# Performance work log

Hardware: AMD Instinct MI355X
Metric: run time of the kernel (lower is better)

Reference implementation:

```python
import jax, jax.numpy as jnp
import numpy as np

N_NODES = 100000


def _gcn_norm(edge_index, num_nodes):
    # PyG GCNConv default: add self-loops, symmetric normalization.
    src, dst = edge_index[0], edge_index[1]
    loop = jnp.arange(num_nodes, dtype=src.dtype)
    src = jnp.concatenate([src, loop])
    dst = jnp.concatenate([dst, loop])
    deg = jax.ops.segment_sum(jnp.ones_like(dst, dtype=jnp.float32), dst,
                              num_segments=num_nodes)
    dinv = jnp.where(deg > 0, jax.lax.rsqrt(jnp.maximum(deg, 1.0)), 0.0)
    norm = dinv[src] * dinv[dst]  # [E + N]
    return src, dst, norm


def _gcn_layer(x, src, dst, norm, W, b, num_nodes):
    h = x @ W                              # [N, out]
    msg = h[src] * norm[:, None]           # gather + scale, [E+N, out]
    agg = jax.ops.segment_sum(msg, dst, num_segments=num_nodes)  # scatter-add
    return agg + b


def setup_inputs() -> dict:
    key = jax.random.key(0)
    ks = jax.random.split(key, 12)
    in_c, hid = 64, 128
    dims = [in_c, hid, hid // 2, hid // 4, hid // 8, 1]
    x = jax.random.normal(ks[0], (N_NODES, in_c), dtype=jnp.float32)
    edge_index = jax.random.randint(ks[1], (2, 1600000), 0, N_NODES,
                                    dtype=jnp.int64)
    inp = {"x": x, "edge_index": edge_index}
    for i in range(5):
        fan_in = dims[i]
        s = 1.0 / np.sqrt(fan_in)
        inp[f"W{i+1}"] = jax.random.uniform(ks[2 + 2 * i], (dims[i], dims[i + 1]),
                                            minval=-s, maxval=s,
                                            dtype=jnp.float32)
        inp[f"b{i+1}"] = jnp.zeros((dims[i + 1],), dtype=jnp.float32)
    return inp


def reference(x, edge_index, W1, b1, W2, b2, W3, b3, W4, b4, W5, b5):
    num_nodes = x.shape[0]
    src, dst, norm = _gcn_norm(edge_index, num_nodes)
    h = _gcn_layer(x, src, dst, norm, W1, b1, num_nodes)
    h = jax.nn.relu(h)
    h = _gcn_layer(h, src, dst, norm, W2, b2, num_nodes)
    h = jax.nn.relu(h)
    h = _gcn_layer(h, src, dst, norm, W3, b3, num_nodes)
    h = jax.nn.relu(h)
    h = _gcn_layer(h, src, dst, norm, W4, b4, num_nodes)
    h = jax.nn.relu(h)
    h = _gcn_layer(h, src, dst, norm, W5, b5, num_nodes)
    return h
```

## Files before the change

kernel.cpp:

```cpp
#include <hip/hip_runtime.h>
#include <math.h>


#define NBIN_MAX 256
#define BSHIFT 9
#define BINW 512
#define CHUNK 2048
#define BCAP 12288

__global__ __launch_bounds__(256) void k_init(int* __restrict__ binCur, int nbin) {
    int t = threadIdx.x;
    if (t < nbin) binCur[t] = t * BCAP;
}

__global__ __launch_bounds__(256) void k_binfill(const int* __restrict__ src,
                                                 const int* __restrict__ dst, int E,
                                                 int nbin, int* __restrict__ binCur,
                                                 unsigned* __restrict__ tmp) {
    __shared__ int h[NBIN_MAX];
    __shared__ int res[NBIN_MAX];
    int t = threadIdx.x;
    int e0 = blockIdx.x * CHUNK;
    int e1 = min(e0 + CHUNK, E);
    int vend = e0 + ((e1 - e0) & ~3);
    for (int i = t; i < nbin; i += 256) h[i] = 0;
    __syncthreads();
    for (int e = e0 + t * 4; e < vend; e += 1024) {
        int4 d = *(const int4*)&dst[e];
        atomicAdd(&h[d.x >> BSHIFT], 1);
        atomicAdd(&h[d.y >> BSHIFT], 1);
        atomicAdd(&h[d.z >> BSHIFT], 1);
        atomicAdd(&h[d.w >> BSHIFT], 1);
    }
    for (int e = vend + t; e < e1; e += 256)
        atomicAdd(&h[dst[e] >> BSHIFT], 1);
    __syncthreads();
    for (int i = t; i < nbin; i += 256)
        res[i] = h[i] ? atomicAdd(&binCur[i], h[i]) : 0;
    __syncthreads();
    for (int i = t; i < nbin; i += 256) h[i] = 0;
    __syncthreads();
    for (int e = e0 + t * 4; e < vend; e += 1024) {
        int4 d = *(const int4*)&dst[e];
        int4 s = *(const int4*)&src[e];
        int b0 = d.x >> BSHIFT;
        int p0 = res[b0] + atomicAdd(&h[b0], 1);
        tmp[p0] = ((unsigned)s.x << BSHIFT) | (unsigned)(d.x & (BINW - 1));
        int b1 = d.y >> BSHIFT;
        int p1 = res[b1] + atomicAdd(&h[b1], 1);
        tmp[p1] = ((unsigned)s.y << BSHIFT) | (unsigned)(d.y & (BINW - 1));
        int b2 = d.z >> BSHIFT;
        int p2 = res[b2] + atomicAdd(&h[b2], 1);
        tmp[p2] = ((unsigned)s.z << BSHIFT) | (unsigned)(d.z & (BINW - 1));
        int b3 = d.w >> BSHIFT;
        int p3 = res[b3] + atomicAdd(&h[b3], 1);
        tmp[p3] = ((unsigned)s.w << BSHIFT) | (unsigned)(d.w & (BINW - 1));
    }
    for (int e = vend + t; e < e1; e += 256) {
        int d = dst[e];
        int b = d >> BSHIFT;
        int p = res[b] + atomicAdd(&h[b], 1);
        tmp[p] = ((unsigned)src[e] << BSHIFT) | (unsigned)(d & (BINW - 1));
    }
}

__global__ __launch_bounds__(256) void k_base(const int* __restrict__ binCur,
                                              int nbin, int* __restrict__ binBase) {
    __shared__ int sh[256];
    int t = threadIdx.x;
    int c = (t < nbin) ? (binCur[t] - t * BCAP) : 0;
    sh[t] = c;
    __syncthreads();
    for (int d = 1; d < 256; d <<= 1) {
        int u = (t >= d) ? sh[t - d] : 0;
        __syncthreads();
        sh[t] += u;
        __syncthreads();
    }
    if (t < nbin) binBase[t] = sh[t] - c;
    if (t == nbin - 1) binBase[nbin] = sh[t];
}

__global__ __launch_bounds__(256) void k_csr(const unsigned* __restrict__ tmp,
                                             const int* __restrict__ binBase,
                                             int n, int nbin,
                                             float* __restrict__ dinv,
                                             int* __restrict__ offs,
                                             int* __restrict__ csr) {
    __shared__ int ldeg[BINW];
    __shared__ int loff[BINW];
    __shared__ int pair[256];
    int b = blockIdx.x;
    int t = threadIdx.x;
    ldeg[t] = 0; ldeg[t + 256] = 0;
    __syncthreads();
    int lo = binBase[b];
    int cnt = binBase[b + 1] - lo;
    const unsigned* tb = tmp + (size_t)b * BCAP;
    for (int p = t; p < cnt; p += 256)
        atomicAdd(&ldeg[tb[p] & (BINW - 1u)], 1);
    __syncthreads();
    int a0 = ldeg[2 * t], a1 = ldeg[2 * t + 1];
    pair[t] = a0 + a1;
    __syncthreads();
    int v = pair[t];
    for (int d = 1; d < 256; d <<= 1) {
        int u = (t >= d) ? pair[t - d] : 0;
        __syncthreads();
        pair[t] += u;
        __syncthreads();
    }
    int ex = pair[t] - v;
    loff[2 * t] = ex;
    loff[2 * t + 1] = ex + a0;
    __syncthreads();
    int v0 = b << BSHIFT;
    for (int i = t; i < BINW; i += 256) {
        int vv = v0 + i;
        if (vv < n) {
            offs[vv] = lo + loff[i];
            dinv[vv] = 1.0f / sqrtf((float)(ldeg[i] + 1));
        }
    }
    if (t == 0 && b == nbin - 1) offs[n] = binBase[nbin];
    __syncthreads();
    ldeg[t] = 0; ldeg[t + 256] = 0;
    __syncthreads();
    for (int p = t; p < cnt; p += 256) {
        unsigned u = tb[p];
        int d0 = (int)(u & (BINW - 1u));
        int pos = loff[d0] + atomicAdd(&ldeg[d0], 1);
        csr[lo + pos] = (int)(u >> BSHIFT);
    }
}

template <int W, int DEPTH, bool RELU, bool BIAS, bool L1S>
__global__ __launch_bounds__(256) void k_aggp(const float* __restrict__ S,
                                              const float* __restrict__ dinv,
                                              const int* __restrict__ offs,
                                              const int* __restrict__ csr,
                                              const float* __restrict__ bg,
                                              float* __restrict__ Y, int n) {
    constexpr int LPR = W / 4;
    constexpr int GPW = 64 / LPR;
    int lane = threadIdx.x & 63;
    int wave = threadIdx.x >> 6;
    int grp = lane / LPR;
    int j = lane % LPR;
    int v = blockIdx.x * (4 * GPW) + wave * GPW + grp;
    if (v >= n) return;
    float dv = dinv[v];
    float4 acc0, acc1 = make_float4(0.f, 0.f, 0.f, 0.f);
    {
        float4 sv = *(const float4*)&S[(size_t)v * W + j * 4];
        float sc = L1S ? dv : 1.0f;
        acc0 = make_float4(sv.x * sc, sv.y * sc, sv.z * sc, sv.w * sc);
    }
    int e0 = offs[v], re = offs[v + 1];
    int nb = (re - e0) / DEPTH;
    float4 bA[DEPTH], bB[DEPTH];
    float dA[DEPTH], dB[DEPTH];
    int iA[DEPTH], iB[DEPTH];
    auto loadIdx = [&](int* ix, int base) {
#pragma unroll
        for (int d = 0; d < DEPTH; ++d)
            ix[d] = __builtin_nontemporal_load(&csr[base + d]);
    };
    auto gather = [&](float4* bf, float* ds, const int* ix) {
#pragma unroll
        for (int d = 0; d < DEPTH; ++d) {
            bf[d] = *(const float4*)&S[(size_t)ix[d] * W + j * 4];
            if (L1S) ds[d] = dinv[ix[d]];
        }
    };
    auto consume = [&](const float4* bf, const float* ds) {
#pragma unroll
        for (int d = 0; d < DEPTH; ++d) {
            float sc = L1S ? ds[d] : 1.0f;
            if (d & 1) { acc1.x += bf[d].x * sc; acc1.y += bf[d].y * sc;
                         acc1.z += bf[d].z * sc; acc1.w += bf[d].w * sc; }
            else       { acc0.x += bf[d].x * sc; acc0.y += bf[d].y * sc;
                         acc0.z += bf[d].z * sc; acc0.w += bf[d].w * sc; }
        }
    };
    if (nb >= 1) {
        loadIdx(iA, e0);
        gather(bA, dA, iA);
        if (nb >= 2) loadIdx(iB, e0 + DEPTH);
        int b = 0;
        while (b + 2 <= nb) {
            gather(bB, dB, iB);
            if (b + 2 < nb) loadIdx(iA, e0 + (b + 2) * DEPTH);
            consume(bA, dA);
            if (b + 2 < nb) {
                gather(bA, dA, iA);
                if (b + 3 < nb) loadIdx(iB, e0 + (b + 3) * DEPTH);
            }
            consume(bB, dB);
            b += 2;
        }
        if (b < nb) consume(bA, dA);
    }
    for (int k = e0 + nb * DEPTH; k < re; ++k) {
        int u = __builtin_nontemporal_load(&csr[k]);
        float4 a = *(const float4*)&S[(size_t)u * W + j * 4];
        float sc = L1S ? dinv[u] : 1.0f;
        acc0.x += a.x * sc; acc0.y += a.y * sc; acc0.z += a.z * sc; acc0.w += a.w * sc;
    }
    acc0.x += acc1.x; acc0.y += acc1.y; acc0.z += acc1.z; acc0.w += acc1.w;
    float4 r;
    r.x = dv * acc0.x; r.y = dv * acc0.y; r.z = dv * acc0.z; r.w = dv * acc0.w;
    if (BIAS) {
        float4 bv = *(const float4*)&bg[j * 4];
        r.x += bv.x; r.y += bv.y; r.z += bv.z; r.w += bv.w;
    }
    if (RELU) {
        r.x = fmaxf(r.x, 0.f); r.y = fmaxf(r.y, 0.f);
        r.z = fmaxf(r.z, 0.f); r.w = fmaxf(r.w, 0.f);
    }
    *(float4*)&Y[(size_t)v * W + j * 4] = r;
}

template <int DEPTH>
__global__ __launch_bounds__(256) void k_agg16g5(const float* __restrict__ S,
                                                 const float* __restrict__ dinv,
                                                 const int* __restrict__ offs,
                                                 const int* __restrict__ csr,
                                                 const float* __restrict__ b4,
                                                 const float* __restrict__ W5,
                                                 float* __restrict__ Y, int n) {
    constexpr int W = 16, LPR = 4, GPW = 16;
    int lane = threadIdx.x & 63;
    int wave = threadIdx.x >> 6;
    int grp = lane / LPR;
    int j = lane % LPR;
    int v = blockIdx.x * (4 * GPW) + wave * GPW + grp;
    if (v >= n) return;
    float dv = dinv[v];
    float4 acc0 = *(const float4*)&S[(size_t)v * W + j * 4];
    float4 acc1 = make_float4(0.f, 0.f, 0.f, 0.f);
    int e0 = offs[v], re = offs[v + 1];
    int nb = (re - e0) / DEPTH;
    float4 bA[DEPTH], bB[DEPTH];
    int iA[DEPTH], iB[DEPTH];
    auto loadIdx = [&](int* ix, int base) {
#pragma unroll
        for (int d = 0; d < DEPTH; ++d)
            ix[d] = __builtin_nontemporal_load(&csr[base + d]);
    };
    auto gather = [&](float4* bf, const int* ix) {
#pragma unroll
        for (int d = 0; d < DEPTH; ++d)
            bf[d] = *(const float4*)&S[(size_t)ix[d] * W + j * 4];
    };
    auto consume = [&](const float4* bf) {
#pragma unroll
        for (int d = 0; d < DEPTH; ++d) {
            if (d & 1) { acc1.x += bf[d].x; acc1.y += bf[d].y;
                         acc1.z += bf[d].z; acc1.w += bf[d].w; }
            else       { acc0.x += bf[d].x; acc0.y += bf[d].y;
                         acc0.z += bf[d].z; acc0.w += bf[d].w; }
        }
    };
    if (nb >= 1) {
        loadIdx(iA, e0);
        gather(bA, iA);
        if (nb >= 2) loadIdx(iB, e0 + DEPTH);
        int b = 0;
        while (b + 2 <= nb) {
            gather(bB, iB);
            if (b + 2 < nb) loadIdx(iA, e0 + (b + 2) * DEPTH);
            consume(bA);
            if (b + 2 < nb) {
                gather(bA, iA);
                if (b + 3 < nb) loadIdx(iB, e0 + (b + 3) * DEPTH);
            }
            consume(bB);
            b += 2;
        }
        if (b < nb) consume(bA);
    }
    for (int k = e0 + nb * DEPTH; k < re; ++k) {
        int u = __builtin_nontemporal_load(&csr[k]);
        float4 a = *(const float4*)&S[(size_t)u * W + j * 4];
        acc0.x += a.x; acc0.y += a.y; acc0.z += a.z; acc0.w += a.w;
    }
    acc0.x += acc1.x; acc0.y += acc1.y; acc0.z += acc1.z; acc0.w += acc1.w;
    float4 bv = *(const float4*)&b4[j * 4];
    float4 w5 = *(const float4*)&W5[j * 4];
    float hx = fmaxf(dv * acc0.x + bv.x, 0.f);
    float hy = fmaxf(dv * acc0.y + bv.y, 0.f);
    float hz = fmaxf(dv * acc0.z + bv.z, 0.f);
    float hw = fmaxf(dv * acc0.w + bv.w, 0.f);
    float p = hx * w5.x + hy * w5.y + hz * w5.z + hw * w5.w;
    p += __shfl_xor(p, 1);
    p += __shfl_xor(p, 2);
    if (j == 0) Y[v] = p * dv;
}

__global__ __launch_bounds__(256) void k_agg1(const float* __restrict__ S,
                                              const float* __restrict__ dinv,
                                              const int* __restrict__ offs,
                                              const int* __restrict__ csr,
                                              const float* __restrict__ bg,
                                              float* __restrict__ Y, int n) {
    int v = blockIdx.x * 256 + threadIdx.x;
    if (v >= n) return;
    float s0 = S[v], s1 = 0.f, s2 = 0.f, s3 = 0.f;
    int e = offs[v], re = offs[v + 1];
    for (; e + 4 <= re; e += 4) {
        int i0 = csr[e], i1 = csr[e + 1], i2 = csr[e + 2], i3 = csr[e + 3];
        s0 += S[i0]; s1 += S[i1]; s2 += S[i2]; s3 += S[i3];
    }
    for (; e < re; ++e) s0 += S[csr[e]];
    Y[v] = dinv[v] * ((s0 + s1) + (s2 + s3)) + bg[0];
}

template <int IN, int OUT, int EPI, int NR>
__global__ __launch_bounds__(256) void k_gemm(const float* __restrict__ X,
                                              const float* __restrict__ Wg,
                                              const float* __restrict__ bg,
                                              const float* __restrict__ dinv,
                                              float* __restrict__ Y, int nrows) {
    constexpr int TPR = OUT / 4;
    constexpr int GROUPS = 256 / TPR;
    constexpr int ROWS = GROUPS * NR;
    constexpr int XS = IN + 1;
    __shared__ __align__(16) float Wl[IN * OUT];
    __shared__ float xl[ROWS * XS];
    __shared__ float bl[OUT];
    int tid = threadIdx.x;
    for (int i = tid; i < IN * OUT; i += 256) Wl[i] = Wg[i];
    if (EPI == 0)
        for (int i = tid; i < OUT; i += 256) bl[i] = bg[i];
    int base = blockIdx.x * ROWS;
    for (int i = tid; i < ROWS * IN; i += 256) {
        int r = i / IN, c = i % IN;
        int row = base + r;
        xl[r * XS + c] = (row < nrows) ? X[(size_t)base * IN + i] : 0.0f;
    }
    __syncthreads();
    int g = tid / TPR;
    int c0 = (tid % TPR) * 4;
    float4 acc[NR];
#pragma unroll
    for (int r = 0; r < NR; ++r) acc[r] = make_float4(0.f, 0.f, 0.f, 0.f);
#pragma unroll 8
    for (int k = 0; k < IN; ++k) {
        float4 w = *(const float4*)&Wl[k * OUT + c0];
#pragma unroll
        for (int r = 0; r < NR; ++r) {
            float a = xl[(g * NR + r) * XS + k];
            acc[r].x += a * w.x; acc[r].y += a * w.y;
            acc[r].z += a * w.z; acc[r].w += a * w.w;
        }
    }
#pragma unroll
    for (int r = 0; r < NR; ++r) {
        int row = base + g * NR + r;
        if (row >= nrows) continue;
        float4 o = acc[r];
        if (EPI == 0) {
            o.x = fmaxf(o.x + bl[c0], 0.f);
            o.y = fmaxf(o.y + bl[c0 + 1], 0.f);
            o.z = fmaxf(o.z + bl[c0 + 2], 0.f);
            o.w = fmaxf(o.w + bl[c0 + 3], 0.f);
        } else {
            float d0 = dinv[row];
            o.x *= d0; o.y *= d0; o.z *= d0; o.w *= d0;
        }
        *(float4*)&Y[(size_t)row * OUT + c0] = o;
    }
}

extern "C" void kernel_launch(void* const* d_in, const int* in_sizes, int n_in,
                              void* d_out, int out_size, void* d_ws, size_t ws_size,
                              hipStream_t stream) {
    const float* x  = (const float*)d_in[0];
    const int*   ei = (const int*)d_in[1];
    const float* W1 = (const float*)d_in[2];  const float* b1 = (const float*)d_in[3];
    const float* W2 = (const float*)d_in[4];  const float* b2 = (const float*)d_in[5];
    const float* W3 = (const float*)d_in[6];  const float* b3 = (const float*)d_in[7];
    const float* W4 = (const float*)d_in[8];  const float* b4 = (const float*)d_in[9];
    const float* W5 = (const float*)d_in[10]; const float* b5 = (const float*)d_in[11];

    const int N = in_sizes[0] / 64;
    const int E = in_sizes[1] / 2;
    const int* src = ei;
    const int* dst = ei + E;
    const int nbin = (N + BINW - 1) / BINW;

    char* ws = (char*)d_ws;
    size_t off = 0;
    auto alloc = [&](size_t bytes) -> void* {
        void* p = ws + off;
        off = (off + bytes + 255) & ~(size_t)255;
        return p;
    };
    float* dinv    = (float*)alloc((size_t)N * 4);
    int*   offs    = (int*)alloc((size_t)(N + 1) * 4);
    int*   binBase = (int*)alloc((size_t)(NBIN_MAX + 1) * 4);
    int*   binCur  = (int*)alloc((size_t)NBIN_MAX * 4);
    int*   csr     = (int*)alloc((size_t)E * 4);
    float* s5      = (float*)alloc((size_t)N * 4);
    float* A       = (float*)alloc((size_t)N * 128 * 4);
    float* B       = (float*)alloc((size_t)N * 64 * 4);
    float* C       = (float*)alloc((size_t)N * 64 * 4);
    unsigned* tmp  = (unsigned*)C;

    k_init<<<1, 256, 0, stream>>>(binCur, nbin);
    k_binfill<<<(E + CHUNK - 1) / CHUNK, 256, 0, stream>>>(src, dst, E, nbin, binCur, tmp);
    k_base<<<1, 256, 0, stream>>>(binCur, nbin, binBase);
    k_csr<<<nbin, 256, 0, stream>>>(tmp, binBase, N, nbin, dinv, offs, csr);

    k_aggp<64, 4, false, false, true><<<(N + 15) / 16, 256, 0, stream>>>(x, dinv, offs, csr, nullptr, B, N);
    k_gemm<64, 128, 0, 4><<<(N + 31) / 32, 256, 0, stream>>>(B, W1, b1, nullptr, A, N);
    k_gemm<128, 64, 1, 2><<<(N + 31) / 32, 256, 0, stream>>>(A, W2, nullptr, dinv, B, N);
    k_aggp<64, 6, true, true, false><<<(N + 15) / 16, 256, 0, stream>>>(B, dinv, offs, csr, b2, C, N);
    k_gemm<64, 32, 1, 2><<<(N + 63) / 64, 256, 0, stream>>>(C, W3, nullptr, dinv, B, N);
    k_aggp<32, 4, true, true, false><<<(N + 31) / 32, 256, 0, stream>>>(B, dinv, offs, csr, b3, A, N);
    k_gemm<32, 16, 1, 2><<<(N + 127) / 128, 256, 0, stream>>>(A, W4, nullptr, dinv, B, N);
    k_agg16g5<4><<<(N + 63) / 64, 256, 0, stream>>>(B, dinv, offs, csr, b4, W5, s5, N);
    k_agg1<<<(N + 255) / 256, 256, 0, stream>>>(s5, dinv, offs, csr, b5, (float*)d_out, N);
}
```

Before: 392.0 us.

## Widen GEMM register tile to 8 columns and vectorize shared-memory loads

The GEMM kernel now has each thread compute 8 output columns instead of 4, which doubles the rows per block and reuses each X value across more FMAs. X rows are read from shared memory as float4 over k, with padding raised to 4. Global-to-shared copies of W and X become float4 loads, and grid sizes are updated to match. The k_aggp template parameter is also changed for two aggregation launches. In exchange, the kernel uses more registers and more shared memory per block, which may lower occupancy.

```diff
diff --git a/kernel.cpp b/kernel.cpp
--- a/kernel.cpp
+++ b/kernel.cpp
@@ -322,54 +322,76 @@
                                               const float* __restrict__ bg,
                                               const float* __restrict__ dinv,
                                               float* __restrict__ Y, int nrows) {
-    constexpr int TPR = OUT / 4;
+    constexpr int TPR = OUT / 8;
     constexpr int GROUPS = 256 / TPR;
     constexpr int ROWS = GROUPS * NR;
-    constexpr int XS = IN + 1;
+    constexpr int XS = IN + 4;
     __shared__ __align__(16) float Wl[IN * OUT];
-    __shared__ float xl[ROWS * XS];
+    __shared__ __align__(16) float xl[ROWS * XS];
     __shared__ float bl[OUT];
     int tid = threadIdx.x;
-    for (int i = tid; i < IN * OUT; i += 256) Wl[i] = Wg[i];
+    for (int i = tid; i < IN * OUT / 4; i += 256)
+        ((float4*)Wl)[i] = ((const float4*)Wg)[i];
     if (EPI == 0)
         for (int i = tid; i < OUT; i += 256) bl[i] = bg[i];
     int base = blockIdx.x * ROWS;
-    for (int i = tid; i < ROWS * IN; i += 256) {
-        int r = i / IN, c = i % IN;
+    for (int i = tid; i < ROWS * (IN / 4); i += 256) {
+        int r = i / (IN / 4), c4 = i % (IN / 4);
         int row = base + r;
-        xl[r * XS + c] = (row < nrows) ? X[(size_t)base * IN + i] : 0.0f;
+        float4 vv = (row < nrows) ? ((const float4*)X)[(size_t)base * (IN / 4) + i]
+                                  : make_float4(0.f, 0.f, 0.f, 0.f);
+        *(float4*)&xl[r * XS + c4 * 4] = vv;
     }
     __syncthreads();
     int g = tid / TPR;
-    int c0 = (tid % TPR) * 4;
-    float4 acc[NR];
-#pragma unroll
-    for (int r = 0; r < NR; ++r) acc[r] = make_float4(0.f, 0.f, 0.f, 0.f);
-#pragma unroll 8
-    for (int k = 0; k < IN; ++k) {
-        float4 w = *(const float4*)&Wl[k * OUT + c0];
-#pragma unroll
-        for (int r = 0; r < NR; ++r) {
-            float a = xl[(g * NR + r) * XS + k];
-            acc[r].x += a * w.x; acc[r].y += a * w.y;
-            acc[r].z += a * w.z; acc[r].w += a * w.w;
+    int c0 = (tid % TPR) * 8;
+    float4 acc[NR][2];
+#pragma unroll
+    for (int r = 0; r < NR; ++r) {
+        acc[r][0] = make_float4(0.f, 0.f, 0.f, 0.f);
+        acc[r][1] = make_float4(0.f, 0.f, 0.f, 0.f);
+    }
+    for (int k4 = 0; k4 < IN; k4 += 4) {
+        float4 a[NR];
+#pragma unroll
+        for (int r = 0; r < NR; ++r)
+            a[r] = *(const float4*)&xl[(g * NR + r) * XS + k4];
+#pragma unroll
+        for (int kk = 0; kk < 4; ++kk) {
+            float4 w0 = *(const float4*)&Wl[(k4 + kk) * OUT + c0];
+            float4 w1 = *(const float4*)&Wl[(k4 + kk) * OUT + c0 + 4];
+#pragma unroll
+            for (int r = 0; r < NR; ++r) {
+                float av = (kk == 0) ? a[r].x : (kk == 1) ? a[r].y
+                         : (kk == 2) ? a[r].z : a[r].w;
+                acc[r][0].x += av * w0.x; acc[r][0].y += av * w0.y;
+                acc[r][0].z += av * w0.z; acc[r][0].w += av * w0.w;
+                acc[r][1].x += av * w1.x; acc[r][1].y += av * w1.y;
+                acc[r][1].z += av * w1.z; acc[r][1].w += av * w1.w;
+            }
         }
     }
 #pragma unroll
     for (int r = 0; r < NR; ++r) {
         int row = base + g * NR + r;
         if (row >= nrows) continue;
-        float4 o = acc[r];
+        float4 o0 = acc[r][0], o1 = acc[r][1];
         if (EPI == 0) {
-            o.x = fmaxf(o.x + bl[c0], 0.f);
-            o.y = fmaxf(o.y + bl[c0 + 1], 0.f);
-            o.z = fmaxf(o.z + bl[c0 + 2], 0.f);
-            o.w = fmaxf(o.w + bl[c0 + 3], 0.f);
+            o0.x = fmaxf(o0.x + bl[c0 + 0], 0.f);
+            o0.y = fmaxf(o0.y + bl[c0 + 1], 0.f);
+            o0.z = fmaxf(o0.z + bl[c0 + 2], 0.f);
+            o0.w = fmaxf(o0.w + bl[c0 + 3], 0.f);
+            o1.x = fmaxf(o1.x + bl[c0 + 4], 0.f);
+            o1.y = fmaxf(o1.y + bl[c0 + 5], 0.f);
+            o1.z = fmaxf(o1.z + bl[c0 + 6], 0.f);
+            o1.w = fmaxf(o1.w + bl[c0 + 7], 0.f);
         } else {
             float d0 = dinv[row];
-            o.x *= d0; o.y *= d0; o.z *= d0; o.w *= d0;
-        }
-        *(float4*)&Y[(size_t)row * OUT + c0] = o;
+            o0.x *= d0; o0.y *= d0; o0.z *= d0; o0.w *= d0;
+            o1.x *= d0; o1.y *= d0; o1.z *= d0; o1.w *= d0;
+        }
+        *(float4*)&Y[(size_t)row * OUT + c0] = o0;
+        *(float4*)&Y[(size_t)row * OUT + c0 + 4] = o1;
     }
 }
 
@@ -413,13 +435,13 @@
     k_base<<<1, 256, 0, stream>>>(binCur, nbin, binBase);
     k_csr<<<nbin, 256, 0, stream>>>(tmp, binBase, N, nbin, dinv, offs, csr);
 
-    k_aggp<64, 4, false, false, true><<<(N + 15) / 16, 256, 0, stream>>>(x, dinv, offs, csr, nullptr, B, N);
-    k_gemm<64, 128, 0, 4><<<(N + 31) / 32, 256, 0, stream>>>(B, W1, b1, nullptr, A, N);
-    k_gemm<128, 64, 1, 2><<<(N + 31) / 32, 256, 0, stream>>>(A, W2, nullptr, dinv, B, N);
-    k_aggp<64, 6, true, true, false><<<(N + 15) / 16, 256, 0, stream>>>(B, dinv, offs, csr, b2, C, N);
-    k_gemm<64, 32, 1, 2><<<(N + 63) / 64, 256, 0, stream>>>(C, W3, nullptr, dinv, B, N);
+    k_aggp<64, 3, false, false, true><<<(N + 15) / 16, 256, 0, stream>>>(x, dinv, offs, csr, nullptr, B, N);
+    k_gemm<64, 128, 0, 4><<<(N + 63) / 64, 256, 0, stream>>>(B, W1, b1, nullptr, A, N);
+    k_gemm<128, 64, 1, 2><<<(N + 63) / 64, 256, 0, stream>>>(A, W2, nullptr, dinv, B, N);
+    k_aggp<64, 4, true, true, false><<<(N + 15) / 16, 256, 0, stream>>>(B, dinv, offs, csr, b2, C, N);
+    k_gemm<64, 32, 1, 2><<<(N + 127) / 128, 256, 0, stream>>>(C, W3, nullptr, dinv, B, N);
     k_aggp<32, 4, true, true, false><<<(N + 31) / 32, 256, 0, stream>>>(B, dinv, offs, csr, b3, A, N);
-    k_gemm<32, 16, 1, 2><<<(N + 127) / 128, 256, 0, stream>>>(A, W4, nullptr, dinv, B, N);
+    k_gemm<32, 16, 1, 2><<<(N + 255) / 256, 256, 0, stream>>>(A, W4, nullptr, dinv, B, N);
     k_agg16g5<4><<<(N + 63) / 64, 256, 0, stream>>>(B, dinv, offs, csr, b4, W5, s5, N);
     k_agg1<<<(N + 255) / 256, 256, 0, stream>>>(s5, dinv, offs, csr, b5, (float*)d_out, N);
 }
```

After: 427.8 us. +9.1%, slower.
